# Optimization experiments

Hardware: AMD Instinct MI355X
Metric: run time of the kernel (lower is better)

Reference implementation:

```python
import jax, jax.numpy as jnp
import numpy as np

SM_SCALE = 0.08838834764831845  # 1/sqrt(128)
SLIDING_WINDOW = 128
N_TOKENS, N_HEADS, Q_MULT, D_HEAD = 2048, 8, 4, 128


def setup_inputs() -> dict:
    key = jax.random.key(0)
    k1, k2, k3, k4 = jax.random.split(key, 4)
    Q = jax.random.normal(k1, (N_TOKENS, N_HEADS, Q_MULT, D_HEAD), dtype=jnp.float32)
    K = jax.random.normal(k2, (N_TOKENS, N_HEADS, D_HEAD), dtype=jnp.float32)
    V = jax.random.normal(k3, (N_TOKENS, N_HEADS, D_HEAD), dtype=jnp.float32)
    S = jax.random.normal(k4, (N_HEADS * Q_MULT,), dtype=jnp.float32)
    return {"Q": Q, "K": K, "V": V, "S": S}


def _build_mask(n_tokens, sliding_window, dtype):
    q_idx = jnp.arange(n_tokens)[:, None]
    k_idx = jnp.arange(n_tokens)[None, :]
    # causal: disallow k > q; sliding window: disallow k <= q - sliding_window
    disallowed = k_idx > q_idx
    if sliding_window > 0:
        disallowed = disallowed | (k_idx <= q_idx - sliding_window)
    return jnp.where(disallowed, jnp.array(-jnp.inf, dtype), jnp.array(0.0, dtype))


def reference(Q, K, V, S):
    n_tokens, n_heads, q_mult, d_head = Q.shape
    mask = _build_mask(n_tokens, SLIDING_WINDOW, Q.dtype)  # (T, T)
    # scores: (h, m, q, k)
    QK = jnp.einsum('qhmd,khd->hmqk', Q, K) * SM_SCALE
    QK = QK + mask[None, None, :, :]
    # append per-(head, q_mult) sink logit as an extra key column
    sink = jnp.broadcast_to(S.reshape(n_heads, q_mult, 1, 1),
                            (n_heads, q_mult, n_tokens, 1))
    QK = jnp.concatenate([QK, sink], axis=-1)  # (h, m, q, k+1)
    W = jax.nn.softmax(QK, axis=-1)[..., :-1]  # drop sink column
    attn = jnp.einsum('hmqk,khd->qhmd', W, V)
    return attn.reshape(n_tokens, n_heads * q_mult * d_head)
```

## Files before the change

### kernel.cpp

```cpp
#include <hip/hip_runtime.h>
#include <cstdint>

#define T_TOK 2048
#define NH 8
#define QM 4
#define DH 128
#define BQ 16
#define PS 40
#define SM_SCALE 0.08838834764831845f

typedef __attribute__((ext_vector_type(8))) short short8v;
typedef __attribute__((ext_vector_type(2))) short short2v;
typedef __attribute__((ext_vector_type(4))) float floatx4;

static __device__ __forceinline__ short f2bf(float x) {
  union { float f; unsigned u; } v; v.f = x;
  return (short)((v.u + 0x7fffu + ((v.u >> 16) & 1u)) >> 16);
}

__global__ __launch_bounds__(256)
void preconvert(const float* __restrict__ K, const float* __restrict__ V,
                short* __restrict__ Kf, short* __restrict__ Vf) {
  __shared__ __align__(16) short lt[64][136];
  const int b = blockIdx.x, t = threadIdx.x;
  const int isK = b < 256 ? 1 : 0;
  const int bb = isK ? b : b - 256;
  const int h = bb & 7, t0 = (bb >> 3) << 6;
  const float* src0 = isK ? K : V;

  {
    const int tt = t >> 2, d0 = (t & 3) * 32;
    const float* src = src0 + ((size_t)(t0 + tt) * NH + h) * DH + d0;
#pragma unroll
    for (int u = 0; u < 8; ++u) {
      float4 x = *(const float4*)(src + 4 * u);
      lt[tt][d0 + 4 * u + 0] = f2bf(x.x);
      lt[tt][d0 + 4 * u + 1] = f2bf(x.y);
      lt[tt][d0 + 4 * u + 2] = f2bf(x.z);
      lt[tt][d0 + 4 * u + 3] = f2bf(x.w);
    }
  }
  __syncthreads();

  const int lane = t & 63, quad = (t >> 4) & 3, l16 = t & 15;
  if (isK) {
    const int s = t >> 6;
#pragma unroll
    for (int T = 0; T < 4; ++T) {
      short8v o = *(const short8v*)(&lt[T * 16 + l16][quad * 8 + s * 32]);
      short* dst = Kf + ((((size_t)h * 128 + (t0 >> 4) + T) * 4 + s) * 64 + lane) * 8;
      *(short8v*)dst = o;
    }
  } else {
    const int grp = t >> 6;
#pragma unroll
    for (int w = 0; w < 4; ++w) {
      const int u = grp + 4 * w;
      const int cp = u >> 3, nt = u & 7;
      short8v o;
#pragma unroll
      for (int j = 0; j < 8; ++j) {
        const int key = quad * 4 + (j >> 1) + 16 * (j & 1);
        o[j] = lt[cp * 32 + key][l16 + 16 * nt];
      }
      short* dst = Vf + ((((size_t)h * 64 + (t0 >> 5) + cp) * 8 + nt) * 64 + lane) * 8;
      *(short8v*)dst = o;
    }
  }
}

__global__ __launch_bounds__(256, 4)
void attn_fwd(const float* __restrict__ Qp, const short* __restrict__ Kf,
              const short* __restrict__ Vf, const float* __restrict__ Sp,
              float* __restrict__ Op) {
  __shared__ __align__(16) short p_s[64 * PS];

  const int t    = threadIdx.x;
  const int lane = t & 63;
  const int wv   = t >> 6;
  const int quad = lane >> 4;
  const int l16  = lane & 15;

  const int bx = blockIdx.x;
  const int h  = bx & 7;
  const int q0 = (bx >> 3) * BQ;
  int lo0 = q0 > 127 ? q0 - 127 : 0;
  lo0 &= ~31;
  const int nk  = q0 + BQ - lo0;
  const int nch = (nk + 31) >> 5;
  const int gc0 = lo0 >> 5;

  const int Ra = wv * 16 + l16;
  const int qa = q0 + (Ra >> 2), ma = Ra & 3;
  const float* qptr = Qp + ((size_t)qa * (NH * QM) + h * QM + ma) * DH + quad * 8;
  short8v qf[4];
#pragma unroll
  for (int s = 0; s < 4; ++s) {
    float4 x0 = *(const float4*)(qptr + 32 * s);
    float4 x1 = *(const float4*)(qptr + 32 * s + 4);
    short8v f;
    f[0] = f2bf(x0.x); f[1] = f2bf(x0.y); f[2] = f2bf(x0.z); f[3] = f2bf(x0.w);
    f[4] = f2bf(x1.x); f[5] = f2bf(x1.y); f[6] = f2bf(x1.z); f[7] = f2bf(x1.w);
    qf[s] = f;
  }

  const int qc = q0 + wv * 4 + quad;
  float dn[4] = {0.f, 0.f, 0.f, 0.f};
  floatx4 oacc[8];
#pragma unroll
  for (int nt = 0; nt < 8; ++nt) oacc[nt] = (floatx4)0.0f;

  const short* kf0 = Kf + (((size_t)h * 128 + 2 * gc0) * 4 * 64 + lane) * 8;
  const short* vf0 = Vf + (((size_t)h * 64 + gc0) * 8 * 64 + lane) * 8;

  for (int c = 0; c < nch; ++c) {
    const int kb = lo0 + c * 32;
    const short* kf = kf0 + (size_t)c * 2 * 4 * 64 * 8;
    const short* vf = vf0 + (size_t)c * 8 * 64 * 8;

    floatx4 sc0 = (floatx4)0.0f, sc1 = (floatx4)0.0f;
#pragma unroll
    for (int s = 0; s < 4; ++s) {
      short8v k0 = *(const short8v*)(kf + s * 512);
      short8v k1 = *(const short8v*)(kf + 2048 + s * 512);
      sc0 = __builtin_amdgcn_mfma_f32_16x16x32_bf16(qf[s], k0, sc0, 0, 0, 0);
      sc1 = __builtin_amdgcn_mfma_f32_16x16x32_bf16(qf[s], k1, sc1, 0, 0, 0);
    }

    const int k0i = kb + l16, k1i = kb + 16 + l16;
    const bool ok0 = (k0i <= qc) && (k0i > qc - 128);
    const bool ok1 = (k1i <= qc) && (k1i > qc - 128);
#pragma unroll
    for (int r = 0; r < 4; ++r) {
      float e0 = ok0 ? __expf(sc0[r] * SM_SCALE) : 0.f;
      float e1 = ok1 ? __expf(sc1[r] * SM_SCALE) : 0.f;
      dn[r] += e0 + e1;
      const int R = wv * 16 + quad * 4 + r;
      short2v p2; p2[0] = f2bf(e0); p2[1] = f2bf(e1);
      *(short2v*)(&p_s[R * PS + 2 * l16]) = p2;
    }
    short8v pf = *(const short8v*)(&p_s[(wv * 16 + l16) * PS + quad * 8]);

#pragma unroll
    for (int nt = 0; nt < 8; ++nt) {
      short8v vfrag = *(const short8v*)(vf + nt * 512);
      oacc[nt] = __builtin_amdgcn_mfma_f32_16x16x32_bf16(pf, vfrag, oacc[nt], 0, 0, 0);
    }
  }

#pragma unroll
  for (int r = 0; r < 4; ++r) {
    float s = dn[r];
#pragma unroll
    for (int mm = 1; mm <= 8; mm <<= 1) s += __shfl_xor(s, mm);
    const float total = s + __expf(Sp[h * QM + r]);
    const float rd = 1.0f / total;
    float* ob = Op + (size_t)qc * (NH * QM * DH) + ((size_t)h * QM + r) * DH + l16;
#pragma unroll
    for (int nt = 0; nt < 8; ++nt) ob[nt * 16] = oacc[nt][r] * rd;
  }
}

extern "C" void kernel_launch(void* const* d_in, const int* in_sizes, int n_in,
                              void* d_out, int out_size, void* d_ws, size_t ws_size,
                              hipStream_t stream) {
  const float* Q = (const float*)d_in[0];
  const float* K = (const float*)d_in[1];
  const float* V = (const float*)d_in[2];
  const float* S = (const float*)d_in[3];
  float* O = (float*)d_out;
  short* Kf = (short*)d_ws;
  short* Vf = Kf + (size_t)8 * 128 * 4 * 64 * 8;

  preconvert<<<dim3(512), dim3(256), 0, stream>>>(K, V, Kf, Vf);
  const int grid = (T_TOK / BQ) * NH;
  attn_fwd<<<dim3(grid), dim3(256), 0, stream>>>(Q, Kf, Vf, S, O);
}
```

Measured before the change: 110.4 us.

## Double query tile per block, stage Q through LDS, reuse K/V fragments

Raises the query block from 16 to 32 tokens so each wave computes two 16-row MFMA tiles against the same K and V fragments, halving K/V global loads per query row. Q is loaded with coalesced float4 reads into a shared-memory staging buffer before being read back as MFMA fragments. The preconvert kernel now writes vectorized short4 stores. The trade-off is more registers and LDS per block, a lowered occupancy hint (2 blocks per CU), and half as many blocks in the grid.

After: 109.0 us. About the same (-1.3%).

```diff
diff --git a/kernel.cpp b/kernel.cpp
--- a/kernel.cpp
+++ b/kernel.cpp
@@ -5,11 +5,13 @@
 #define NH 8
 #define QM 4
 #define DH 128
-#define BQ 16
+#define BQ 32
+#define QS 136
 #define PS 40
 #define SM_SCALE 0.08838834764831845f
 
 typedef __attribute__((ext_vector_type(8))) short short8v;
+typedef __attribute__((ext_vector_type(4))) short short4v;
 typedef __attribute__((ext_vector_type(2))) short short2v;
 typedef __attribute__((ext_vector_type(4))) float floatx4;
 
@@ -34,10 +36,9 @@
 #pragma unroll
     for (int u = 0; u < 8; ++u) {
       float4 x = *(const float4*)(src + 4 * u);
-      lt[tt][d0 + 4 * u + 0] = f2bf(x.x);
-      lt[tt][d0 + 4 * u + 1] = f2bf(x.y);
-      lt[tt][d0 + 4 * u + 2] = f2bf(x.z);
-      lt[tt][d0 + 4 * u + 3] = f2bf(x.w);
+      short4v s4;
+      s4[0] = f2bf(x.x); s4[1] = f2bf(x.y); s4[2] = f2bf(x.z); s4[3] = f2bf(x.w);
+      *(short4v*)(&lt[tt][d0 + 4 * u]) = s4;
     }
   }
   __syncthreads();
@@ -69,11 +70,12 @@
   }
 }
 
-__global__ __launch_bounds__(256, 4)
+__global__ __launch_bounds__(256, 2)
 void attn_fwd(const float* __restrict__ Qp, const short* __restrict__ Kf,
               const short* __restrict__ Vf, const float* __restrict__ Sp,
               float* __restrict__ Op) {
-  __shared__ __align__(16) short p_s[64 * PS];
+  __shared__ __align__(16) short q_s[128 * QS];
+  __shared__ __align__(16) short p_s[128 * PS];
 
   const int t    = threadIdx.x;
   const int lane = t & 63;
@@ -88,76 +90,101 @@
   lo0 &= ~31;
   const int nk  = q0 + BQ - lo0;
   const int nch = (nk + 31) >> 5;
-  const int gc0 = lo0 >> 5;
-
-  const int Ra = wv * 16 + l16;
-  const int qa = q0 + (Ra >> 2), ma = Ra & 3;
-  const float* qptr = Qp + ((size_t)qa * (NH * QM) + h * QM + ma) * DH + quad * 8;
-  short8v qf[4];
-#pragma unroll
-  for (int s = 0; s < 4; ++s) {
-    float4 x0 = *(const float4*)(qptr + 32 * s);
-    float4 x1 = *(const float4*)(qptr + 32 * s + 4);
-    short8v f;
-    f[0] = f2bf(x0.x); f[1] = f2bf(x0.y); f[2] = f2bf(x0.z); f[3] = f2bf(x0.w);
-    f[4] = f2bf(x1.x); f[5] = f2bf(x1.y); f[6] = f2bf(x1.z); f[7] = f2bf(x1.w);
-    qf[s] = f;
-  }
-
-  const int qc = q0 + wv * 4 + quad;
-  float dn[4] = {0.f, 0.f, 0.f, 0.f};
-  floatx4 oacc[8];
-#pragma unroll
-  for (int nt = 0; nt < 8; ++nt) oacc[nt] = (floatx4)0.0f;
-
-  const short* kf0 = Kf + (((size_t)h * 128 + 2 * gc0) * 4 * 64 + lane) * 8;
-  const short* vf0 = Vf + (((size_t)h * 64 + gc0) * 8 * 64 + lane) * 8;
+
+  {
+    const float* qsrc = Qp + ((size_t)q0 * 32 + h * 4) * 128;
+#pragma unroll
+    for (int p = 0; p < 16; ++p) {
+      const int g = t + p * 256;
+      const int seg = g >> 7, w = g & 127;
+      const float4 x = *(const float4*)(qsrc + (size_t)seg * 4096 + w * 4);
+      short4v s4;
+      s4[0] = f2bf(x.x); s4[1] = f2bf(x.y); s4[2] = f2bf(x.z); s4[3] = f2bf(x.w);
+      *(short4v*)(&q_s[(seg * 4 + (w >> 5)) * QS + (w & 31) * 4]) = s4;
+    }
+  }
+  __syncthreads();
+
+  short8v qf[2][4];
+#pragma unroll
+  for (int T = 0; T < 2; ++T)
+#pragma unroll
+    for (int s = 0; s < 4; ++s)
+      qf[T][s] = *(const short8v*)(&q_s[(wv * 32 + T * 16 + l16) * QS + quad * 8 + 32 * s]);
+
+  float dn[2][4];
+#pragma unroll
+  for (int T = 0; T < 2; ++T)
+#pragma unroll
+    for (int r = 0; r < 4; ++r) dn[T][r] = 0.f;
+  floatx4 oacc[2][8];
+#pragma unroll
+  for (int T = 0; T < 2; ++T)
+#pragma unroll
+    for (int nt = 0; nt < 8; ++nt) oacc[T][nt] = (floatx4)0.0f;
+
+  const short* kfb = Kf + (((size_t)h * 128 + (lo0 >> 4)) * 4 * 64 + lane) * 8;
+  const short* vfb = Vf + (((size_t)h * 64 + (lo0 >> 5)) * 8 * 64 + lane) * 8;
 
   for (int c = 0; c < nch; ++c) {
     const int kb = lo0 + c * 32;
-    const short* kf = kf0 + (size_t)c * 2 * 4 * 64 * 8;
-    const short* vf = vf0 + (size_t)c * 8 * 64 * 8;
-
-    floatx4 sc0 = (floatx4)0.0f, sc1 = (floatx4)0.0f;
+    const short* kf = kfb + (size_t)c * 4096;
+    const short* vf = vfb + (size_t)c * 4096;
+
+    floatx4 sc[2][2];
+    sc[0][0] = (floatx4)0.0f; sc[0][1] = (floatx4)0.0f;
+    sc[1][0] = (floatx4)0.0f; sc[1][1] = (floatx4)0.0f;
 #pragma unroll
     for (int s = 0; s < 4; ++s) {
       short8v k0 = *(const short8v*)(kf + s * 512);
       short8v k1 = *(const short8v*)(kf + 2048 + s * 512);
-      sc0 = __builtin_amdgcn_mfma_f32_16x16x32_bf16(qf[s], k0, sc0, 0, 0, 0);
-      sc1 = __builtin_amdgcn_mfma_f32_16x16x32_bf16(qf[s], k1, sc1, 0, 0, 0);
+      sc[0][0] = __builtin_amdgcn_mfma_f32_16x16x32_bf16(qf[0][s], k0, sc[0][0], 0, 0, 0);
+      sc[0][1] = __builtin_amdgcn_mfma_f32_16x16x32_bf16(qf[0][s], k1, sc[0][1], 0, 0, 0);
+      sc[1][0] = __builtin_amdgcn_mfma_f32_16x16x32_bf16(qf[1][s], k0, sc[1][0], 0, 0, 0);
+      sc[1][1] = __builtin_amdgcn_mfma_f32_16x16x32_bf16(qf[1][s], k1, sc[1][1], 0, 0, 0);
     }
 
     const int k0i = kb + l16, k1i = kb + 16 + l16;
-    const bool ok0 = (k0i <= qc) && (k0i > qc - 128);
-    const bool ok1 = (k1i <= qc) && (k1i > qc - 128);
+#pragma unroll
+    for (int T = 0; T < 2; ++T) {
+      const int qc = q0 + 8 * wv + 4 * T + quad;
+      const bool ok0 = (k0i <= qc) && (k0i > qc - 128);
+      const bool ok1 = (k1i <= qc) && (k1i > qc - 128);
+      const int Rb = wv * 32 + T * 16 + quad * 4;
+#pragma unroll
+      for (int r = 0; r < 4; ++r) {
+        float e0 = ok0 ? __expf(sc[T][0][r] * SM_SCALE) : 0.f;
+        float e1 = ok1 ? __expf(sc[T][1][r] * SM_SCALE) : 0.f;
+        dn[T][r] += e0 + e1;
+        short2v p2; p2[0] = f2bf(e0); p2[1] = f2bf(e1);
+        *(short2v*)(&p_s[(Rb + r) * PS + 2 * l16]) = p2;
+      }
+    }
+
+    short8v pf0 = *(const short8v*)(&p_s[(wv * 32 + l16) * PS + quad * 8]);
+    short8v pf1 = *(const short8v*)(&p_s[(wv * 32 + 16 + l16) * PS + quad * 8]);
+#pragma unroll
+    for (int nt = 0; nt < 8; ++nt) {
+      short8v vfr = *(const short8v*)(vf + nt * 512);
+      oacc[0][nt] = __builtin_amdgcn_mfma_f32_16x16x32_bf16(pf0, vfr, oacc[0][nt], 0, 0, 0);
+      oacc[1][nt] = __builtin_amdgcn_mfma_f32_16x16x32_bf16(pf1, vfr, oacc[1][nt], 0, 0, 0);
+    }
+  }
+
+#pragma unroll
+  for (int T = 0; T < 2; ++T) {
+    const int qc = q0 + 8 * wv + 4 * T + quad;
 #pragma unroll
     for (int r = 0; r < 4; ++r) {
-      float e0 = ok0 ? __expf(sc0[r] * SM_SCALE) : 0.f;
-      float e1 = ok1 ? __expf(sc1[r] * SM_SCALE) : 0.f;
-      dn[r] += e0 + e1;
-      const int R = wv * 16 + quad * 4 + r;
-      short2v p2; p2[0] = f2bf(e0); p2[1] = f2bf(e1);
-      *(short2v*)(&p_s[R * PS + 2 * l16]) = p2;
-    }
-    short8v pf = *(const short8v*)(&p_s[(wv * 16 + l16) * PS + quad * 8]);
-
-#pragma unroll
-    for (int nt = 0; nt < 8; ++nt) {
-      short8v vfrag = *(const short8v*)(vf + nt * 512);
-      oacc[nt] = __builtin_amdgcn_mfma_f32_16x16x32_bf16(pf, vfrag, oacc[nt], 0, 0, 0);
-    }
-  }
-
-#pragma unroll
-  for (int r = 0; r < 4; ++r) {
-    float s = dn[r];
-#pragma unroll
-    for (int mm = 1; mm <= 8; mm <<= 1) s += __shfl_xor(s, mm);
-    const float total = s + __expf(Sp[h * QM + r]);
-    const float rd = 1.0f / total;
-    float* ob = Op + (size_t)qc * (NH * QM * DH) + ((size_t)h * QM + r) * DH + l16;
-#pragma unroll
-    for (int nt = 0; nt < 8; ++nt) ob[nt * 16] = oacc[nt][r] * rd;
+      float s = dn[T][r];
+#pragma unroll
+      for (int mm = 1; mm <= 8; mm <<= 1) s += __shfl_xor(s, mm);
+      const float total = s + __expf(Sp[h * QM + r]);
+      const float rd = 1.0f / total;
+      float* ob = Op + (size_t)qc * 4096 + (h * 4 + r) * 128 + l16;
+#pragma unroll
+      for (int nt = 0; nt < 8; ++nt) ob[nt * 16] = oacc[T][nt][r] * rd;
+    }
   }
 }
 
```
